# Kernel tuning notes

Hardware: AMD Instinct MI355X
Metric: run time of the kernel (lower is better)

## Reference

```python
import jax, jax.numpy as jnp
import numpy as np

DIM = 1024
NUM_EXPERTS = 8
TOP_K = 2
B, S = 2, 2048
HID = 4 * DIM


def setup_inputs() -> dict:
    key = jax.random.key(0)
    ks = jax.random.split(key, 7)
    scale = 0.02
    x = jax.random.normal(ks[0], (B, S, DIM), dtype=jnp.float32)
    gate_w = jax.random.normal(ks[1], (DIM, NUM_EXPERTS), dtype=jnp.float32) * scale
    gate_b = jnp.zeros((NUM_EXPERTS,), dtype=jnp.float32)
    w1 = jax.random.normal(ks[2], (NUM_EXPERTS, DIM, HID), dtype=jnp.float32) * scale
    b1 = jnp.zeros((NUM_EXPERTS, HID), dtype=jnp.float32)
    w2 = jax.random.normal(ks[3], (NUM_EXPERTS, HID, DIM), dtype=jnp.float32) * scale
    b2 = jnp.zeros((NUM_EXPERTS, DIM), dtype=jnp.float32)
    return {"x": x, "gate_w": gate_w, "gate_b": gate_b,
            "w1": w1, "b1": b1, "w2": w2, "b2": b2}


def reference(x, gate_w, gate_b, w1, b1, w2, b2):
    # Gate: [B,S,E]
    gates = jnp.einsum('bsd,de->bse', x, gate_w) + gate_b
    top_w, top_idx = jax.lax.top_k(gates, TOP_K)          # [B,S,K]
    probs = jax.nn.softmax(top_w, axis=-1)                # softmax over selected logits
    # Dense all-expert FFN (matches original: every expert runs on every token)
    h = jnp.einsum('bsd,edh->bseh', x, w1) + b1           # [B,S,E,4D]
    h = jax.nn.gelu(h, approximate=False)                 # exact GELU (torch default)
    y = jnp.einsum('bseh,ehd->bsed', h, w2) + b2          # [B,S,E,D]
    # Select top-k experts per token and combine
    sel = jnp.take_along_axis(y, top_idx[..., None], axis=2)   # [B,S,K,D]
    return jnp.sum(sel * probs[..., None], axis=2)        # [B,S,D]
```

## Files before the change

### kernel.cpp

```cpp
#include <hip/hip_runtime.h>
#include <hip/hip_bf16.h>

#define T_TOKENS 4096
#define DIM      1024
#define HID      4096
#define NE       8
#define CAP      4096
#define SPLITS   2
#define KSP      (HID / SPLITS)

typedef __attribute__((ext_vector_type(8))) short  bf16x8;
typedef __attribute__((ext_vector_type(4))) float  f32x4;
typedef __attribute__((ext_vector_type(4))) ushort u16x4;

__device__ static inline ushort f2bf(float f) {
    __hip_bfloat16 h = __float2bfloat16(f);
    return *(ushort*)&h;
}

__device__ static inline void gll16(const void* g, void* l) {
    __builtin_amdgcn_global_load_lds(
        (const __attribute__((address_space(1))) void*)g,
        (__attribute__((address_space(3))) void*)l,
        16, 0, 0);
}

#define MFMA16(a, b, c) __builtin_amdgcn_mfma_f32_16x16x32_bf16((a), (b), (c), 0, 0, 0)

__global__ __launch_bounds__(64) void gate_kernel(
    const float* __restrict__ x, const float* __restrict__ gw,
    const float* __restrict__ gb, __hip_bfloat16* __restrict__ xb,
    int* __restrict__ counts, int* __restrict__ tlist, float* __restrict__ plist)
{
    const int tok = blockIdx.x;
    const int l   = threadIdx.x;
    const float* xr = x + (size_t)tok * DIM;

    float part[NE];
#pragma unroll
    for (int e = 0; e < NE; e++) part[e] = 0.f;

#pragma unroll
    for (int i = 0; i < DIM / 64; i++) {
        int d = i * 64 + l;
        float xv = xr[d];
        xb[(size_t)tok * DIM + d] = __float2bfloat16(xv);
        const float4* g4 = (const float4*)(gw + (size_t)d * NE);
        float4 a = g4[0], b = g4[1];
        part[0] += xv * a.x; part[1] += xv * a.y;
        part[2] += xv * a.z; part[3] += xv * a.w;
        part[4] += xv * b.x; part[5] += xv * b.y;
        part[6] += xv * b.z; part[7] += xv * b.w;
    }
#pragma unroll
    for (int off = 32; off > 0; off >>= 1) {
#pragma unroll
        for (int e = 0; e < NE; e++) part[e] += __shfl_xor(part[e], off, 64);
    }
    if (l == 0) {
        float lg[NE];
#pragma unroll
        for (int e = 0; e < NE; e++) lg[e] = part[e] + gb[e];
        int i0 = 0;
#pragma unroll
        for (int e = 1; e < NE; e++) if (lg[e] > lg[i0]) i0 = e;
        int i1 = (i0 == 0) ? 1 : 0;
#pragma unroll
        for (int e = 0; e < NE; e++) if (e != i0 && lg[e] > lg[i1]) i1 = e;
        float t  = expf(lg[i1] - lg[i0]);
        float p0 = 1.f / (1.f + t);
        float p1 = t / (1.f + t);
        int pos0 = atomicAdd(&counts[i0], 1);
        tlist[i0 * CAP + pos0] = tok; plist[i0 * CAP + pos0] = p0;
        int pos1 = atomicAdd(&counts[i1], 1);
        tlist[i1 * CAP + pos1] = tok; plist[i1 * CAP + pos1] = p1;
    }
}

__global__ void finalize_kernel(const int* __restrict__ counts, int* __restrict__ base)
{
    if (threadIdx.x == 0) {
        int acc = 0;
        for (int e = 0; e < NE; e++) { base[e] = acc; acc += counts[e]; }
        base[NE] = acc;
    }
}

__global__ __launch_bounds__(256) void transpose_cvt64(
    const float* __restrict__ in, __hip_bfloat16* __restrict__ outp, int K, int N)
{
    __shared__ ushort tile[64][68];
    const int e  = blockIdx.z;
    const float* src = in + (size_t)e * K * N;
    ushort* dst = (ushort*)outp + (size_t)e * K * N;
    const int k0 = blockIdx.y * 64, n0 = blockIdx.x * 64;
    const int tid = threadIdx.x;

    const int rn4 = (tid & 15) * 4;
    const int rk  = tid >> 4;
#pragma unroll
    for (int p = 0; p < 4; p++) {
        int k = rk + p * 16;
        float4 v = *(const float4*)&src[(size_t)(k0 + k) * N + n0 + rn4];
        tile[k][rn4 + 0] = f2bf(v.x);
        tile[k][rn4 + 1] = f2bf(v.y);
        tile[k][rn4 + 2] = f2bf(v.z);
        tile[k][rn4 + 3] = f2bf(v.w);
    }
    __syncthreads();
    const int wk4 = (tid & 15) * 4;
    const int wn  = tid >> 4;
#pragma unroll
    for (int p = 0; p < 4; p++) {
        int n = wn + p * 16;
        u16x4 u;
        u[0] = tile[wk4 + 0][n];
        u[1] = tile[wk4 + 1][n];
        u[2] = tile[wk4 + 2][n];
        u[3] = tile[wk4 + 3][n];
        *(u16x4*)&dst[(size_t)(n0 + n) * K + k0 + wk4] = u;
    }
}


#define AOFFc(d,s) (((d)*2+(s))*8192)
#define BOFFc(d,s) (32768 + ((d)*2+(s))*8192)

#define MFMA_CL(nj0, nj1)                                                    \
    _Pragma("unroll")                                                        \
    for (int mi = 0; mi < 8; mi++) {                                         \
        acc[mi][nj0] = MFMA16(af[mi], bf##nj0, acc[mi][nj0]);                \
        acc[mi][nj1] = MFMA16(af[mi], bf##nj1, acc[mi][nj1]);                \
    }

#define GEMM_CORE(NT, srcA0, srcA1, srcB0, srcB1)                            \
    f32x4 acc[8][4];                                                         \
    _Pragma("unroll")                                                        \
    for (int i = 0; i < 8; i++)                                              \
        _Pragma("unroll")                                                    \
        for (int j = 0; j < 4; j++) acc[i][j] = (f32x4){0.f,0.f,0.f,0.f};    \
    const int lm = l & 15, kg = l >> 4;                                      \
    const int rch = (kg ^ ((lm >> 1) & 3)) * 8;                              \
    const int a0 = (wr * 128 + lm) * 32 + rch;                               \
    const int b0 = (wc * 64 + lm) * 32 + rch;                                \
                \
    gll16(srcA0,      &lds[AOFFc(0,0) + w*512]);                             \
    gll16(srcA1,      &lds[AOFFc(0,0) + 4096 + w*512]);                      \
    gll16(srcB0,      &lds[BOFFc(0,0) + w*512]);                             \
    gll16(srcB1,      &lds[BOFFc(0,0) + 4096 + w*512]);                      \
    gll16(srcA0 + 32, &lds[AOFFc(0,1) + w*512]);                             \
    gll16(srcA1 + 32, &lds[AOFFc(0,1) + 4096 + w*512]);                      \
    gll16(srcB0 + 32, &lds[BOFFc(0,1) + w*512]);                             \
    gll16(srcB1 + 32, &lds[BOFFc(0,1) + 4096 + w*512]);                      \
    asm volatile("s_waitcnt vmcnt(4)" ::: "memory");                         \
    gll16(srcA0 + 64, &lds[AOFFc(1,0) + w*512]);                             \
    gll16(srcA1 + 64, &lds[AOFFc(1,0) + 4096 + w*512]);                      \
    gll16(srcB0 + 64, &lds[BOFFc(1,0) + w*512]);                             \
    gll16(srcB1 + 64, &lds[BOFFc(1,0) + 4096 + w*512]);                      \
    gll16(srcA0 + 96, &lds[AOFFc(1,1) + w*512]);                             \
    gll16(srcA1 + 96, &lds[AOFFc(1,1) + 4096 + w*512]);                      \
    asm volatile("s_waitcnt vmcnt(6)" ::: "memory");                         \
    __builtin_amdgcn_s_barrier();                                            \
    _Pragma("unroll 1")                                                      \
    for (int t = 0; t < NT; t++) {                                           \
        const int d   = t & 1;                                               \
        const int aof  = d * 16384,        bof  = 32768 + d * 16384;         \
        const int aofN = (d^1) * 16384,    bofN = 32768 + (d^1) * 16384;     \
        bf16x8 af[8]; bf16x8 bf0, bf1, bf2, bf3;                             \
                \
        _Pragma("unroll")                                                    \
        for (int mi = 0; mi < 8; mi++)                                       \
            af[mi] = *(const bf16x8*)&lds[aof + a0 + mi*512];                \
        bf0 = *(const bf16x8*)&lds[bof + b0];                                \
        bf1 = *(const bf16x8*)&lds[bof + b0 + 512];                          \
        if (t + 1 < NT) {                                                    \
            size_t ko = (size_t)(t+1)*64 + 32;                               \
            gll16(srcB0 + ko, &lds[bofN + 8192 + w*512]);                    \
            gll16(srcB1 + ko, &lds[bofN + 8192 + 4096 + w*512]);             \
        }                                                                    \
        __builtin_amdgcn_s_barrier();                                        \
        __builtin_amdgcn_s_setprio(1);                                       \
        MFMA_CL(0, 1)                                                        \
        __builtin_amdgcn_s_setprio(0);                                       \
        __builtin_amdgcn_s_barrier();                                        \
                          \
        bf2 = *(const bf16x8*)&lds[bof + b0 + 1024];                         \
        bf3 = *(const bf16x8*)&lds[bof + b0 + 1536];                         \
        if (t + 2 < NT) {                                                    \
            size_t ko = (size_t)(t+2)*64;                                    \
            gll16(srcA0 + ko, &lds[aof + w*512]);                            \
            gll16(srcA1 + ko, &lds[aof + 4096 + w*512]);                     \
        }                                                                    \
        __builtin_amdgcn_s_barrier();                                        \
        __builtin_amdgcn_s_setprio(1);                                       \
        MFMA_CL(2, 3)                                                        \
        __builtin_amdgcn_s_setprio(0);                                       \
        __builtin_amdgcn_s_barrier();                                        \
                \
        _Pragma("unroll")                                                    \
        for (int mi = 0; mi < 8; mi++)                                       \
            af[mi] = *(const bf16x8*)&lds[aof + 8192 + a0 + mi*512];         \
        bf0 = *(const bf16x8*)&lds[bof + 8192 + b0];                         \
        bf1 = *(const bf16x8*)&lds[bof + 8192 + b0 + 512];                   \
        if (t + 2 < NT) {                                                    \
            size_t ko = (size_t)(t+2)*64;                                    \
            gll16(srcB0 + ko, &lds[bof + w*512]);                            \
            gll16(srcB1 + ko, &lds[bof + 4096 + w*512]);                     \
        }                                                                    \
        __builtin_amdgcn_s_barrier();                                        \
        __builtin_amdgcn_s_setprio(1);                                       \
        MFMA_CL(0, 1)                                                        \
        __builtin_amdgcn_s_setprio(0);                                       \
        __builtin_amdgcn_s_barrier();                                        \
            \
        bf2 = *(const bf16x8*)&lds[bof + 8192 + b0 + 1024];                  \
        bf3 = *(const bf16x8*)&lds[bof + 8192 + b0 + 1536];                  \
        if (t + 2 < NT) {                                                    \
            size_t ko = (size_t)(t+2)*64 + 32;                               \
            gll16(srcA0 + ko, &lds[aof + 8192 + w*512]);                     \
            gll16(srcA1 + ko, &lds[aof + 8192 + 4096 + w*512]);              \
        }                                                                    \
        __builtin_amdgcn_s_barrier();                                        \
        __builtin_amdgcn_s_setprio(1);                                       \
        MFMA_CL(2, 3)                                                        \
        __builtin_amdgcn_s_setprio(0);                                       \
        if (t < NT - 2) { asm volatile("s_waitcnt vmcnt(6)" ::: "memory"); } \
        else            { asm volatile("s_waitcnt vmcnt(0)" ::: "memory"); } \
        __builtin_amdgcn_s_barrier();                                        \
    }

__global__ __launch_bounds__(512, 2) void ffn1_kernel(
    const __hip_bfloat16* __restrict__ xb, const __hip_bfloat16* __restrict__ w1t,
    const float* __restrict__ b1, const int* __restrict__ counts,
    const int* __restrict__ base, const int* __restrict__ tlist,
    __hip_bfloat16* __restrict__ H)
{
    const int e  = blockIdx.z;
    const int ne = counts[e];
    const int rb = blockIdx.y, cb = blockIdx.x;
    if (rb * 256 >= ne) return;

    __shared__ __align__(16) ushort lds[65536];

    const int tid = threadIdx.x;
    const int l = tid & 63, w = tid >> 6;
    const int wr = w >> 2, wc = w & 3;

    const int srow = tid >> 2;
    const int sch  = tid & 3;
    const int sc0  = (sch ^ ((srow >> 1) & 3)) * 8;
    const int rA0g = rb * 256 + srow;
    const int rA1g = rA0g + 128;
    const int tok0 = tlist[e * CAP + (rA0g < ne ? rA0g : ne - 1)];
    const int tok1 = tlist[e * CAP + (rA1g < ne ? rA1g : ne - 1)];
    const ushort* srcA0 = (const ushort*)xb + (size_t)tok0 * DIM + sc0;
    const ushort* srcA1 = (const ushort*)xb + (size_t)tok1 * DIM + sc0;
    const ushort* srcB0 = (const ushort*)w1t + ((size_t)e * HID + cb * 256 + srow) * DIM + sc0;
    const ushort* srcB1 = srcB0 + (size_t)128 * DIM;

    GEMM_CORE(16, srcA0, srcA1, srcB0, srcB1)

    const int hb = base[e];
#pragma unroll
    for (int nj = 0; nj < 4; nj++) {
        int col = cb * 256 + wc * 64 + nj * 16 + lm;
        float bias = b1[e * HID + col];
#pragma unroll
        for (int mi = 0; mi < 8; mi++) {
#pragma unroll
            for (int jj = 0; jj < 4; jj++) {
                int r = rb * 256 + wr * 128 + mi * 16 + kg * 4 + jj;
                if (r < ne) {
                    float v = acc[mi][nj][jj] + bias;
                    v = 0.5f * v * (1.0f + erff(v * 0.70710678118654752f));
                    H[(size_t)(hb + r) * HID + col] = __float2bfloat16(v);
                }
            }
        }
    }
}

__global__ __launch_bounds__(512, 2) void ffn2_kernel(
    const __hip_bfloat16* __restrict__ H, const __hip_bfloat16* __restrict__ w2t,
    const float* __restrict__ b2, const int* __restrict__ counts,
    const int* __restrict__ base, const int* __restrict__ tlist,
    const float* __restrict__ plist, float* __restrict__ out)
{
    const int e  = blockIdx.z;
    const int ne = counts[e];
    const int rb = blockIdx.y >> 1;
    const int sp = blockIdx.y & 1;
    const int cb = blockIdx.x;
    if (rb * 256 >= ne) return;

    __shared__ __align__(16) ushort lds[65536];

    const int tid = threadIdx.x;
    const int l = tid & 63, w = tid >> 6;
    const int wr = w >> 2, wc = w & 3;

    const int srow = tid >> 2;
    const int sch  = tid & 3;
    const int sc0  = (sch ^ ((srow >> 1) & 3)) * 8;
    const int hb   = base[e];
    const int rA0g = rb * 256 + srow;
    const int rA1g = rA0g + 128;
    const int hr0  = hb + (rA0g < ne ? rA0g : ne - 1);
    const int hr1  = hb + (rA1g < ne ? rA1g : ne - 1);
    const size_t ko0 = (size_t)sp * KSP;
    const ushort* srcA0 = (const ushort*)H + (size_t)hr0 * HID + ko0 + sc0;
    const ushort* srcA1 = (const ushort*)H + (size_t)hr1 * HID + ko0 + sc0;
    const ushort* srcB0 = (const ushort*)w2t + ((size_t)e * DIM + cb * 256 + srow) * HID + ko0 + sc0;
    const ushort* srcB1 = srcB0 + (size_t)128 * HID;

    GEMM_CORE(32, srcA0, srcA1, srcB0, srcB1)

#pragma unroll
    for (int mi = 0; mi < 8; mi++) {
#pragma unroll
        for (int jj = 0; jj < 4; jj++) {
            int r = rb * 256 + wr * 128 + mi * 16 + kg * 4 + jj;
            if (r < ne) {
                int tok = tlist[e * CAP + r];
                float p = plist[e * CAP + r];
                float* orow = out + (size_t)tok * DIM;
#pragma unroll
                for (int nj = 0; nj < 4; nj++) {
                    int col = cb * 256 + wc * 64 + nj * 16 + lm;
                    float v = acc[mi][nj][jj];
                    if (sp == 0) v += b2[e * DIM + col];
                    unsafeAtomicAdd(&orow[col], v * p);
                }
            }
        }
    }
}

extern "C" void kernel_launch(void* const* d_in, const int* in_sizes, int n_in,
                              void* d_out, int out_size, void* d_ws, size_t ws_size,
                              hipStream_t stream)
{
    const float* x  = (const float*)d_in[0];
    const float* gw = (const float*)d_in[1];
    const float* gb = (const float*)d_in[2];
    const float* w1 = (const float*)d_in[3];
    const float* b1 = (const float*)d_in[4];
    const float* w2 = (const float*)d_in[5];
    const float* b2 = (const float*)d_in[6];
    float* out = (float*)d_out;

    char* ws = (char*)d_ws;
    __hip_bfloat16* w1t = (__hip_bfloat16*)(ws);
    __hip_bfloat16* w2t = (__hip_bfloat16*)(ws + 67108864);
    __hip_bfloat16* Hb  = (__hip_bfloat16*)(ws + 134217728);
    __hip_bfloat16* xb  = (__hip_bfloat16*)(ws + 201326592);
    int*   tlist  = (int*)  (ws + 209715200);
    float* plist  = (float*)(ws + 209846272);
    int*   counts = (int*)  (ws + 209977344);
    int*   basep  = (int*)  (ws + 209977408);

    hipMemsetAsync(out, 0, (size_t)T_TOKENS * DIM * sizeof(float), stream);
    hipMemsetAsync(counts, 0, 64, stream);

    gate_kernel<<<T_TOKENS, 64, 0, stream>>>(x, gw, gb, xb, counts, tlist, plist);
    finalize_kernel<<<1, 64, 0, stream>>>(counts, basep);

    transpose_cvt64<<<dim3(HID / 64, DIM / 64, NE), 256, 0, stream>>>(w1, w1t, DIM, HID);
    transpose_cvt64<<<dim3(DIM / 64, HID / 64, NE), 256, 0, stream>>>(w2, w2t, HID, DIM);

    ffn1_kernel<<<dim3(HID / 256, CAP / 256, NE), 512, 0, stream>>>(
        xb, w1t, b1, counts, basep, tlist, Hb);
    ffn2_kernel<<<dim3(DIM / 256, (CAP / 256) * SPLITS, NE), 512, 0, stream>>>(
        Hb, w2t, b2, counts, basep, tlist, plist, out);
}
```

Before: 543.1 us.

## Replace sparse expert grids with persistent kernels pulling compacted task lists

The finalize kernel now builds compact task lists of (expert, row-block, column-block) tiles for both FFN GEMMs. The FFN kernels become persistent 256-block kernels that claim tiles from these lists through an atomic ticket counter. This removes the many early-exit blocks that the padded CAP-sized grid launched and is meant to balance work across CUs. The cost is two barriers and one atomic per tile, and dynamic ordering that may hurt cache locality.

```diff
diff --git a/kernel.cpp b/kernel.cpp
--- a/kernel.cpp
+++ b/kernel.cpp
@@ -77,12 +77,33 @@
     }
 }
 
-__global__ void finalize_kernel(const int* __restrict__ counts, int* __restrict__ base)
-{
+__global__ void finalize_kernel(const int* __restrict__ counts, int* __restrict__ base,
+                                int* __restrict__ task1, int* __restrict__ task2,
+                                int* __restrict__ ntasks)
+{
+    __shared__ int stc[NE], so1[NE], so2[NE];
     if (threadIdx.x == 0) {
-        int acc = 0;
-        for (int e = 0; e < NE; e++) { base[e] = acc; acc += counts[e]; }
+        int acc = 0, o1 = 0, o2 = 0;
+        for (int e = 0; e < NE; e++) {
+            base[e] = acc; acc += counts[e];
+            int tc = (counts[e] + 255) >> 8;
+            stc[e] = tc; so1[e] = o1; so2[e] = o2;
+            o1 += tc * 16; o2 += tc * 8;
+        }
         base[NE] = acc;
+        ntasks[0] = o1; ntasks[1] = o2;
+    }
+    __syncthreads();
+    for (int e = 0; e < NE; e++) {
+        int tc = stc[e];
+        for (int i = threadIdx.x; i < tc * 16; i += 64) {
+            int rb = i >> 4, cb = i & 15;
+            task1[so1[e] + i] = (e << 16) | (rb << 8) | cb;
+        }
+        for (int i = threadIdx.x; i < tc * 8; i += 64) {
+            int rb = i >> 3, c = i & 7;
+            task2[so2[e] + i] = (e << 16) | (rb << 8) | c;
+        }
     }
 }
 
@@ -139,8 +160,6 @@
     for (int i = 0; i < 8; i++)                                              \
         _Pragma("unroll")                                                    \
         for (int j = 0; j < 4; j++) acc[i][j] = (f32x4){0.f,0.f,0.f,0.f};    \
-    const int lm = l & 15, kg = l >> 4;                                      \
-    const int rch = (kg ^ ((lm >> 1) & 3)) * 8;                              \
     const int a0 = (wr * 128 + lm) * 32 + rch;                               \
     const int b0 = (wc * 64 + lm) * 32 + rch;                                \
                 \
@@ -233,47 +252,58 @@
     const __hip_bfloat16* __restrict__ xb, const __hip_bfloat16* __restrict__ w1t,
     const float* __restrict__ b1, const int* __restrict__ counts,
     const int* __restrict__ base, const int* __restrict__ tlist,
-    __hip_bfloat16* __restrict__ H)
-{
-    const int e  = blockIdx.z;
-    const int ne = counts[e];
-    const int rb = blockIdx.y, cb = blockIdx.x;
-    if (rb * 256 >= ne) return;
-
+    const int* __restrict__ task1, const int* __restrict__ ntasks,
+    int* __restrict__ ticket, __hip_bfloat16* __restrict__ H)
+{
     __shared__ __align__(16) ushort lds[65536];
+    __shared__ int s_task;
 
     const int tid = threadIdx.x;
     const int l = tid & 63, w = tid >> 6;
     const int wr = w >> 2, wc = w & 3;
-
+    const int lm = l & 15, kg = l >> 4;
+    const int rch = (kg ^ ((lm >> 1) & 3)) * 8;
     const int srow = tid >> 2;
     const int sch  = tid & 3;
     const int sc0  = (sch ^ ((srow >> 1) & 3)) * 8;
-    const int rA0g = rb * 256 + srow;
-    const int rA1g = rA0g + 128;
-    const int tok0 = tlist[e * CAP + (rA0g < ne ? rA0g : ne - 1)];
-    const int tok1 = tlist[e * CAP + (rA1g < ne ? rA1g : ne - 1)];
-    const ushort* srcA0 = (const ushort*)xb + (size_t)tok0 * DIM + sc0;
-    const ushort* srcA1 = (const ushort*)xb + (size_t)tok1 * DIM + sc0;
-    const ushort* srcB0 = (const ushort*)w1t + ((size_t)e * HID + cb * 256 + srow) * DIM + sc0;
-    const ushort* srcB1 = srcB0 + (size_t)128 * DIM;
-
-    GEMM_CORE(16, srcA0, srcA1, srcB0, srcB1)
-
-    const int hb = base[e];
-#pragma unroll
-    for (int nj = 0; nj < 4; nj++) {
-        int col = cb * 256 + wc * 64 + nj * 16 + lm;
-        float bias = b1[e * HID + col];
-#pragma unroll
-        for (int mi = 0; mi < 8; mi++) {
-#pragma unroll
-            for (int jj = 0; jj < 4; jj++) {
-                int r = rb * 256 + wr * 128 + mi * 16 + kg * 4 + jj;
-                if (r < ne) {
-                    float v = acc[mi][nj][jj] + bias;
-                    v = 0.5f * v * (1.0f + erff(v * 0.70710678118654752f));
-                    H[(size_t)(hb + r) * HID + col] = __float2bfloat16(v);
+    const int nt1  = ntasks[0];
+
+    for (;;) {
+        __syncthreads();
+        if (tid == 0) s_task = atomicAdd(ticket, 1);
+        __syncthreads();
+        const int task = s_task;
+        if (task >= nt1) break;
+        const int v  = task1[task];
+        const int e  = v >> 16, rb = (v >> 8) & 255, cb = v & 255;
+        const int ne = counts[e];
+
+        const int rA0g = rb * 256 + srow;
+        const int rA1g = rA0g + 128;
+        const int tok0 = tlist[e * CAP + (rA0g < ne ? rA0g : ne - 1)];
+        const int tok1 = tlist[e * CAP + (rA1g < ne ? rA1g : ne - 1)];
+        const ushort* srcA0 = (const ushort*)xb + (size_t)tok0 * DIM + sc0;
+        const ushort* srcA1 = (const ushort*)xb + (size_t)tok1 * DIM + sc0;
+        const ushort* srcB0 = (const ushort*)w1t + ((size_t)e * HID + cb * 256 + srow) * DIM + sc0;
+        const ushort* srcB1 = srcB0 + (size_t)128 * DIM;
+
+        GEMM_CORE(16, srcA0, srcA1, srcB0, srcB1)
+
+        const int hb = base[e];
+#pragma unroll
+        for (int nj = 0; nj < 4; nj++) {
+            int col = cb * 256 + wc * 64 + nj * 16 + lm;
+            float bias = b1[e * HID + col];
+#pragma unroll
+            for (int mi = 0; mi < 8; mi++) {
+#pragma unroll
+                for (int jj = 0; jj < 4; jj++) {
+                    int r = rb * 256 + wr * 128 + mi * 16 + kg * 4 + jj;
+                    if (r < ne) {
+                        float vv = acc[mi][nj][jj] + bias;
+                        vv = 0.5f * vv * (1.0f + erff(vv * 0.70710678118654752f));
+                        H[(size_t)(hb + r) * HID + col] = __float2bfloat16(vv);
+                    }
                 }
             }
         }
@@ -284,52 +314,63 @@
     const __hip_bfloat16* __restrict__ H, const __hip_bfloat16* __restrict__ w2t,
     const float* __restrict__ b2, const int* __restrict__ counts,
     const int* __restrict__ base, const int* __restrict__ tlist,
-    const float* __restrict__ plist, float* __restrict__ out)
-{
-    const int e  = blockIdx.z;
-    const int ne = counts[e];
-    const int rb = blockIdx.y >> 1;
-    const int sp = blockIdx.y & 1;
-    const int cb = blockIdx.x;
-    if (rb * 256 >= ne) return;
-
+    const float* __restrict__ plist, const int* __restrict__ task2,
+    const int* __restrict__ ntasks, int* __restrict__ ticket,
+    float* __restrict__ out)
+{
     __shared__ __align__(16) ushort lds[65536];
+    __shared__ int s_task;
 
     const int tid = threadIdx.x;
     const int l = tid & 63, w = tid >> 6;
     const int wr = w >> 2, wc = w & 3;
-
+    const int lm = l & 15, kg = l >> 4;
+    const int rch = (kg ^ ((lm >> 1) & 3)) * 8;
     const int srow = tid >> 2;
     const int sch  = tid & 3;
     const int sc0  = (sch ^ ((srow >> 1) & 3)) * 8;
-    const int hb   = base[e];
-    const int rA0g = rb * 256 + srow;
-    const int rA1g = rA0g + 128;
-    const int hr0  = hb + (rA0g < ne ? rA0g : ne - 1);
-    const int hr1  = hb + (rA1g < ne ? rA1g : ne - 1);
-    const size_t ko0 = (size_t)sp * KSP;
-    const ushort* srcA0 = (const ushort*)H + (size_t)hr0 * HID + ko0 + sc0;
-    const ushort* srcA1 = (const ushort*)H + (size_t)hr1 * HID + ko0 + sc0;
-    const ushort* srcB0 = (const ushort*)w2t + ((size_t)e * DIM + cb * 256 + srow) * HID + ko0 + sc0;
-    const ushort* srcB1 = srcB0 + (size_t)128 * HID;
-
-    GEMM_CORE(32, srcA0, srcA1, srcB0, srcB1)
-
-#pragma unroll
-    for (int mi = 0; mi < 8; mi++) {
-#pragma unroll
-        for (int jj = 0; jj < 4; jj++) {
-            int r = rb * 256 + wr * 128 + mi * 16 + kg * 4 + jj;
-            if (r < ne) {
-                int tok = tlist[e * CAP + r];
-                float p = plist[e * CAP + r];
-                float* orow = out + (size_t)tok * DIM;
-#pragma unroll
-                for (int nj = 0; nj < 4; nj++) {
-                    int col = cb * 256 + wc * 64 + nj * 16 + lm;
-                    float v = acc[mi][nj][jj];
-                    if (sp == 0) v += b2[e * DIM + col];
-                    unsafeAtomicAdd(&orow[col], v * p);
+    const int nt2  = ntasks[1];
+
+    for (;;) {
+        __syncthreads();
+        if (tid == 0) s_task = atomicAdd(ticket, 1);
+        __syncthreads();
+        const int task = s_task;
+        if (task >= nt2) break;
+        const int v  = task2[task];
+        const int e  = v >> 16, rb = (v >> 8) & 255;
+        const int cb = (v & 255) >> 1, sp = v & 1;
+        const int ne = counts[e];
+        const int hb = base[e];
+
+        const int rA0g = rb * 256 + srow;
+        const int rA1g = rA0g + 128;
+        const int hr0  = hb + (rA0g < ne ? rA0g : ne - 1);
+        const int hr1  = hb + (rA1g < ne ? rA1g : ne - 1);
+        const size_t ko0 = (size_t)sp * KSP;
+        const ushort* srcA0 = (const ushort*)H + (size_t)hr0 * HID + ko0 + sc0;
+        const ushort* srcA1 = (const ushort*)H + (size_t)hr1 * HID + ko0 + sc0;
+        const ushort* srcB0 = (const ushort*)w2t + ((size_t)e * DIM + cb * 256 + srow) * HID + ko0 + sc0;
+        const ushort* srcB1 = srcB0 + (size_t)128 * HID;
+
+        GEMM_CORE(32, srcA0, srcA1, srcB0, srcB1)
+
+#pragma unroll
+        for (int mi = 0; mi < 8; mi++) {
+#pragma unroll
+            for (int jj = 0; jj < 4; jj++) {
+                int r = rb * 256 + wr * 128 + mi * 16 + kg * 4 + jj;
+                if (r < ne) {
+                    int tok = tlist[e * CAP + r];
+                    float p = plist[e * CAP + r];
+                    float* orow = out + (size_t)tok * DIM;
+#pragma unroll
+                    for (int nj = 0; nj < 4; nj++) {
+                        int col = cb * 256 + wc * 64 + nj * 16 + lm;
+                        float vv = acc[mi][nj][jj];
+                        if (sp == 0) vv += b2[e * DIM + col];
+                        unsafeAtomicAdd(&orow[col], vv * p);
+                    }
                 }
             }
         }
@@ -358,18 +399,22 @@
     float* plist  = (float*)(ws + 209846272);
     int*   counts = (int*)  (ws + 209977344);
     int*   basep  = (int*)  (ws + 209977408);
+    int*   ntasks = (int*)  (ws + 209977472);
+    int*   tickets= (int*)  (ws + 209977536);
+    int*   task1  = (int*)  (ws + 209977600);
+    int*   task2  = (int*)  (ws + 209985792);
 
     hipMemsetAsync(out, 0, (size_t)T_TOKENS * DIM * sizeof(float), stream);
-    hipMemsetAsync(counts, 0, 64, stream);
+    hipMemsetAsync(counts, 0, 256, stream);
 
     gate_kernel<<<T_TOKENS, 64, 0, stream>>>(x, gw, gb, xb, counts, tlist, plist);
-    finalize_kernel<<<1, 64, 0, stream>>>(counts, basep);
+    finalize_kernel<<<1, 64, 0, stream>>>(counts, basep, task1, task2, ntasks);
 
     transpose_cvt64<<<dim3(HID / 64, DIM / 64, NE), 256, 0, stream>>>(w1, w1t, DIM, HID);
     transpose_cvt64<<<dim3(DIM / 64, HID / 64, NE), 256, 0, stream>>>(w2, w2t, HID, DIM);
 
-    ffn1_kernel<<<dim3(HID / 256, CAP / 256, NE), 512, 0, stream>>>(
-        xb, w1t, b1, counts, basep, tlist, Hb);
-    ffn2_kernel<<<dim3(DIM / 256, (CAP / 256) * SPLITS, NE), 512, 0, stream>>>(
-        Hb, w2t, b2, counts, basep, tlist, plist, out);
-}
+    ffn1_kernel<<<256, 512, 0, stream>>>(
+        xb, w1t, b1, counts, basep, tlist, task1, ntasks, &tickets[0], Hb);
+    ffn2_kernel<<<256, 512, 0, stream>>>(
+        Hb, w2t, b2, counts, basep, tlist, plist, task2, ntasks, &tickets[1], out);
+}
```

Measured after the change: 541.6 us. Within noise of the previous version (-0.3%).

## Convert FFN GEMMs to persistent per-expert grids with strided task loops

Applied to the files above, without the earlier changes.

Replaces the sparse 3D grids in the two expert GEMM kernels, where many blocks exit early, with 256 persistent blocks. Each expert gets 32 blocks that loop over that expert's row×column (and K-split) tiles. Launch bounds drop to one block per CU. This is meant to remove wasted block launches and balance work across CUs. The risk is load imbalance between experts with very different token counts, since the fixed assignment of 32 blocks per expert leaves some blocks idle.

```diff
diff --git a/kernel.cpp b/kernel.cpp
--- a/kernel.cpp
+++ b/kernel.cpp
@@ -139,11 +139,8 @@
     for (int i = 0; i < 8; i++)                                              \
         _Pragma("unroll")                                                    \
         for (int j = 0; j < 4; j++) acc[i][j] = (f32x4){0.f,0.f,0.f,0.f};    \
-    const int lm = l & 15, kg = l >> 4;                                      \
-    const int rch = (kg ^ ((lm >> 1) & 3)) * 8;                              \
     const int a0 = (wr * 128 + lm) * 32 + rch;                               \
     const int b0 = (wc * 64 + lm) * 32 + rch;                                \
-                \
     gll16(srcA0,      &lds[AOFFc(0,0) + w*512]);                             \
     gll16(srcA1,      &lds[AOFFc(0,0) + 4096 + w*512]);                      \
     gll16(srcB0,      &lds[BOFFc(0,0) + w*512]);                             \
@@ -165,9 +162,8 @@
     for (int t = 0; t < NT; t++) {                                           \
         const int d   = t & 1;                                               \
         const int aof  = d * 16384,        bof  = 32768 + d * 16384;         \
-        const int aofN = (d^1) * 16384,    bofN = 32768 + (d^1) * 16384;     \
+        const int bofN = 32768 + (d^1) * 16384;                              \
         bf16x8 af[8]; bf16x8 bf0, bf1, bf2, bf3;                             \
-                \
         _Pragma("unroll")                                                    \
         for (int mi = 0; mi < 8; mi++)                                       \
             af[mi] = *(const bf16x8*)&lds[aof + a0 + mi*512];                \
@@ -183,7 +179,6 @@
         MFMA_CL(0, 1)                                                        \
         __builtin_amdgcn_s_setprio(0);                                       \
         __builtin_amdgcn_s_barrier();                                        \
-                          \
         bf2 = *(const bf16x8*)&lds[bof + b0 + 1024];                         \
         bf3 = *(const bf16x8*)&lds[bof + b0 + 1536];                         \
         if (t + 2 < NT) {                                                    \
@@ -196,7 +191,6 @@
         MFMA_CL(2, 3)                                                        \
         __builtin_amdgcn_s_setprio(0);                                       \
         __builtin_amdgcn_s_barrier();                                        \
-                \
         _Pragma("unroll")                                                    \
         for (int mi = 0; mi < 8; mi++)                                       \
             af[mi] = *(const bf16x8*)&lds[aof + 8192 + a0 + mi*512];         \
@@ -212,7 +206,6 @@
         MFMA_CL(0, 1)                                                        \
         __builtin_amdgcn_s_setprio(0);                                       \
         __builtin_amdgcn_s_barrier();                                        \
-            \
         bf2 = *(const bf16x8*)&lds[bof + 8192 + b0 + 1024];                  \
         bf3 = *(const bf16x8*)&lds[bof + 8192 + b0 + 1536];                  \
         if (t + 2 < NT) {                                                    \
@@ -229,107 +222,122 @@
         __builtin_amdgcn_s_barrier();                                        \
     }
 
-__global__ __launch_bounds__(512, 2) void ffn1_kernel(
+__global__ __launch_bounds__(512, 1) void ffn1_kernel(
     const __hip_bfloat16* __restrict__ xb, const __hip_bfloat16* __restrict__ w1t,
     const float* __restrict__ b1, const int* __restrict__ counts,
     const int* __restrict__ base, const int* __restrict__ tlist,
     __hip_bfloat16* __restrict__ H)
 {
-    const int e  = blockIdx.z;
+    __shared__ __align__(16) ushort lds[65536];
+
+    const int e  = blockIdx.x & 7;
+    const int cu = blockIdx.x >> 3;
     const int ne = counts[e];
-    const int rb = blockIdx.y, cb = blockIdx.x;
-    if (rb * 256 >= ne) return;
-
-    __shared__ __align__(16) ushort lds[65536];
+    const int tc = (ne + 255) >> 8;
+    const int ntask = tc * 16;
 
     const int tid = threadIdx.x;
     const int l = tid & 63, w = tid >> 6;
     const int wr = w >> 2, wc = w & 3;
-
+    const int lm = l & 15, kg = l >> 4;
+    const int rch = (kg ^ ((lm >> 1) & 3)) * 8;
     const int srow = tid >> 2;
     const int sch  = tid & 3;
     const int sc0  = (sch ^ ((srow >> 1) & 3)) * 8;
-    const int rA0g = rb * 256 + srow;
-    const int rA1g = rA0g + 128;
-    const int tok0 = tlist[e * CAP + (rA0g < ne ? rA0g : ne - 1)];
-    const int tok1 = tlist[e * CAP + (rA1g < ne ? rA1g : ne - 1)];
-    const ushort* srcA0 = (const ushort*)xb + (size_t)tok0 * DIM + sc0;
-    const ushort* srcA1 = (const ushort*)xb + (size_t)tok1 * DIM + sc0;
-    const ushort* srcB0 = (const ushort*)w1t + ((size_t)e * HID + cb * 256 + srow) * DIM + sc0;
-    const ushort* srcB1 = srcB0 + (size_t)128 * DIM;
-
-    GEMM_CORE(16, srcA0, srcA1, srcB0, srcB1)
-
     const int hb = base[e];
-#pragma unroll
-    for (int nj = 0; nj < 4; nj++) {
-        int col = cb * 256 + wc * 64 + nj * 16 + lm;
-        float bias = b1[e * HID + col];
-#pragma unroll
-        for (int mi = 0; mi < 8; mi++) {
-#pragma unroll
-            for (int jj = 0; jj < 4; jj++) {
-                int r = rb * 256 + wr * 128 + mi * 16 + kg * 4 + jj;
-                if (r < ne) {
-                    float v = acc[mi][nj][jj] + bias;
-                    v = 0.5f * v * (1.0f + erff(v * 0.70710678118654752f));
-                    H[(size_t)(hb + r) * HID + col] = __float2bfloat16(v);
+
+    for (int i = cu; i < ntask; i += 32) {
+        const int rb = i >> 4, cb = i & 15;
+        __syncthreads();
+
+        const int rA0g = rb * 256 + srow;
+        const int rA1g = rA0g + 128;
+        const int tok0 = tlist[e * CAP + (rA0g < ne ? rA0g : ne - 1)];
+        const int tok1 = tlist[e * CAP + (rA1g < ne ? rA1g : ne - 1)];
+        const ushort* srcA0 = (const ushort*)xb + (size_t)tok0 * DIM + sc0;
+        const ushort* srcA1 = (const ushort*)xb + (size_t)tok1 * DIM + sc0;
+        const ushort* srcB0 = (const ushort*)w1t + ((size_t)e * HID + cb * 256 + srow) * DIM + sc0;
+        const ushort* srcB1 = srcB0 + (size_t)128 * DIM;
+
+        GEMM_CORE(16, srcA0, srcA1, srcB0, srcB1)
+
+#pragma unroll
+        for (int nj = 0; nj < 4; nj++) {
+            int col = cb * 256 + wc * 64 + nj * 16 + lm;
+            float bias = b1[e * HID + col];
+#pragma unroll
+            for (int mi = 0; mi < 8; mi++) {
+#pragma unroll
+                for (int jj = 0; jj < 4; jj++) {
+                    int r = rb * 256 + wr * 128 + mi * 16 + kg * 4 + jj;
+                    if (r < ne) {
+                        float vv = acc[mi][nj][jj] + bias;
+                        vv = 0.5f * vv * (1.0f + erff(vv * 0.70710678118654752f));
+                        H[(size_t)(hb + r) * HID + col] = __float2bfloat16(vv);
+                    }
                 }
             }
         }
     }
 }
 
-__global__ __launch_bounds__(512, 2) void ffn2_kernel(
+__global__ __launch_bounds__(512, 1) void ffn2_kernel(
     const __hip_bfloat16* __restrict__ H, const __hip_bfloat16* __restrict__ w2t,
     const float* __restrict__ b2, const int* __restrict__ counts,
     const int* __restrict__ base, const int* __restrict__ tlist,
     const float* __restrict__ plist, float* __restrict__ out)
 {
-    const int e  = blockIdx.z;
+    __shared__ __align__(16) ushort lds[65536];
+
+    const int e  = blockIdx.x & 7;
+    const int cu = blockIdx.x >> 3;
     const int ne = counts[e];
-    const int rb = blockIdx.y >> 1;
-    const int sp = blockIdx.y & 1;
-    const int cb = blockIdx.x;
-    if (rb * 256 >= ne) return;
-
-    __shared__ __align__(16) ushort lds[65536];
+    const int tc = (ne + 255) >> 8;
+    const int ntask = tc * 8;
+    const int hb = base[e];
 
     const int tid = threadIdx.x;
     const int l = tid & 63, w = tid >> 6;
     const int wr = w >> 2, wc = w & 3;
-
+    const int lm = l & 15, kg = l >> 4;
+    const int rch = (kg ^ ((lm >> 1) & 3)) * 8;
     const int srow = tid >> 2;
     const int sch  = tid & 3;
     const int sc0  = (sch ^ ((srow >> 1) & 3)) * 8;
-    const int hb   = base[e];
-    const int rA0g = rb * 256 + srow;
-    const int rA1g = rA0g + 128;
-    const int hr0  = hb + (rA0g < ne ? rA0g : ne - 1);
-    const int hr1  = hb + (rA1g < ne ? rA1g : ne - 1);
-    const size_t ko0 = (size_t)sp * KSP;
-    const ushort* srcA0 = (const ushort*)H + (size_t)hr0 * HID + ko0 + sc0;
-    const ushort* srcA1 = (const ushort*)H + (size_t)hr1 * HID + ko0 + sc0;
-    const ushort* srcB0 = (const ushort*)w2t + ((size_t)e * DIM + cb * 256 + srow) * HID + ko0 + sc0;
-    const ushort* srcB1 = srcB0 + (size_t)128 * HID;
-
-    GEMM_CORE(32, srcA0, srcA1, srcB0, srcB1)
-
-#pragma unroll
-    for (int mi = 0; mi < 8; mi++) {
-#pragma unroll
-        for (int jj = 0; jj < 4; jj++) {
-            int r = rb * 256 + wr * 128 + mi * 16 + kg * 4 + jj;
-            if (r < ne) {
-                int tok = tlist[e * CAP + r];
-                float p = plist[e * CAP + r];
-                float* orow = out + (size_t)tok * DIM;
-#pragma unroll
-                for (int nj = 0; nj < 4; nj++) {
-                    int col = cb * 256 + wc * 64 + nj * 16 + lm;
-                    float v = acc[mi][nj][jj];
-                    if (sp == 0) v += b2[e * DIM + col];
-                    unsafeAtomicAdd(&orow[col], v * p);
+
+    for (int i = cu; i < ntask; i += 32) {
+        const int rb = i >> 3;
+        const int cb = (i >> 1) & 3, sp = i & 1;
+        __syncthreads();
+
+        const int rA0g = rb * 256 + srow;
+        const int rA1g = rA0g + 128;
+        const int hr0  = hb + (rA0g < ne ? rA0g : ne - 1);
+        const int hr1  = hb + (rA1g < ne ? rA1g : ne - 1);
+        const size_t ko0 = (size_t)sp * KSP;
+        const ushort* srcA0 = (const ushort*)H + (size_t)hr0 * HID + ko0 + sc0;
+        const ushort* srcA1 = (const ushort*)H + (size_t)hr1 * HID + ko0 + sc0;
+        const ushort* srcB0 = (const ushort*)w2t + ((size_t)e * DIM + cb * 256 + srow) * HID + ko0 + sc0;
+        const ushort* srcB1 = srcB0 + (size_t)128 * HID;
+
+        GEMM_CORE(32, srcA0, srcA1, srcB0, srcB1)
+
+#pragma unroll
+        for (int mi = 0; mi < 8; mi++) {
+#pragma unroll
+            for (int jj = 0; jj < 4; jj++) {
+                int r = rb * 256 + wr * 128 + mi * 16 + kg * 4 + jj;
+                if (r < ne) {
+                    int tok = tlist[e * CAP + r];
+                    float p = plist[e * CAP + r];
+                    float* orow = out + (size_t)tok * DIM;
+#pragma unroll
+                    for (int nj = 0; nj < 4; nj++) {
+                        int col = cb * 256 + wc * 64 + nj * 16 + lm;
+                        float vv = acc[mi][nj][jj];
+                        if (sp == 0) vv += b2[e * DIM + col];
+                        unsafeAtomicAdd(&orow[col], vv * p);
+                    }
                 }
             }
         }
@@ -368,8 +376,8 @@
     transpose_cvt64<<<dim3(HID / 64, DIM / 64, NE), 256, 0, stream>>>(w1, w1t, DIM, HID);
     transpose_cvt64<<<dim3(DIM / 64, HID / 64, NE), 256, 0, stream>>>(w2, w2t, HID, DIM);
 
-    ffn1_kernel<<<dim3(HID / 256, CAP / 256, NE), 512, 0, stream>>>(
+    ffn1_kernel<<<256, 512, 0, stream>>>(
         xb, w1t, b1, counts, basep, tlist, Hb);
-    ffn2_kernel<<<dim3(DIM / 256, (CAP / 256) * SPLITS, NE), 512, 0, stream>>>(
+    ffn2_kernel<<<256, 512, 0, stream>>>(
         Hb, w2t, b2, counts, basep, tlist, plist, out);
 }
```

After: 535.6 us. No clear change (-1.4%).
